# Optimization experiments

Hardware: AMD Instinct MI355X
Metric: run time of the kernel (lower is better)

## Reference

```python
import jax, jax.numpy as jnp
import numpy as np

IN_FF = 7  # joints
MASK = np.ones(9, dtype=np.float32)  # [P(3), RPY sin/cos (6)]


def _mlp(x, params):
    # params: list of (W, b); sigmoid after every layer except the last (predict)
    h = x
    for W, b in params[:-1]:
        h = jax.nn.sigmoid(h @ W + b)
    W, b = params[-1]
    return h @ W + b


def _rpy_head(x, params):
    # FeedForwardNet_RPY forward: y -> [sin(y0), cos(y1)], angle = atan2(sin, cos)
    y = _mlp(x, params)
    s = jnp.sin(y[..., 0])
    c = jnp.cos(y[..., 1])
    ang = jnp.arctan2(s, c)
    return jnp.stack([s, c, ang], axis=-1)  # (..., 3)


def setup_inputs():
    key = jax.random.key(0)
    ks = jax.random.split(key, 26)
    m = 16384
    d = {"x": jax.random.normal(ks[0], (m, 2 * IN_FF), jnp.float32)}

    def lin(k, fi, fo, name, i):
        k1, k2 = jax.random.split(k)
        lim = 1.0 / np.sqrt(fi)  # torch Linear default init
        d[name + "_W" + str(i)] = jax.random.uniform(k1, (fi, fo), jnp.float32, -lim, lim)
        d[name + "_b" + str(i)] = jax.random.uniform(k2, (fo,), jnp.float32, -lim, lim)

    idx = 1
    for name, dims in [("pos", [7, 512, 512, 3]), ("roll", [7, 256, 256, 2]),
                       ("pitch", [7, 256, 256, 2]), ("yaw", [7, 256, 256, 2])]:
        for i in range(3):
            lin(ks[idx], dims[i], dims[i + 1], name, i)
            idx += 1
    return d


def _forward(x, pos_p, roll_p, pitch_p, yaw_p):
    mask = jnp.asarray(MASK)
    M_P, M_RPY = mask[:3], mask[3:]
    q, qdot = x[:, :IN_FF], x[:, IN_FF:]

    # position net: forward + per-sample Jacobian (exact, replaces the autograd loop)
    P = _mlp(q, pos_p)                                          # (m, 3)
    J_P = jax.vmap(jax.jacfwd(lambda z: _mlp(z, pos_p)))(q)     # (m, 3, 7)
    vel = jnp.einsum("moi,mi->mo", J_P, qdot)                   # bmm(J_P, jointVels)
    P = P * M_P
    vel = vel * M_P

    heads = []
    for p in (roll_p, pitch_p, yaw_p):
        f = lambda z, p=p: _rpy_head(z, p)
        y = f(q)                                # (m, 3): [sin, cos, angle]
        J = jax.vmap(jax.jacfwd(f))(q)          # (m, 3, 7)
        v = jnp.einsum("moi,mi->mo", J[:, :2, :], qdot)  # (m, 2)
        heads.append((y, J, v))
    (yR, JR, vR), (yPi, JPi, vPi), (yY, JY, vY) = heads

    # order: [roll_sin, pitch_sin, yaw_sin, roll_cos, pitch_cos, yaw_cos]
    RPY = jnp.stack([yR[:, 0], yPi[:, 0], yY[:, 0], yR[:, 1], yPi[:, 1], yY[:, 1]], axis=1) * M_RPY
    vel_RPY = jnp.stack([vR[:, 0], vPi[:, 0], vY[:, 0], vR[:, 1], vPi[:, 1], vY[:, 1]], axis=1) * M_RPY
    J_RPY = jnp.stack([JR[:, 0], JPi[:, 0], JY[:, 0], JR[:, 1], JPi[:, 1], JY[:, 1]], axis=1)  # (m,6,7)

    out = jnp.concatenate([P, RPY, vel, vel_RPY], axis=1)            # (m, 18)
    J_tot = jnp.concatenate([J_P, J_RPY], axis=1)                    # (m, 9, 7)
    out_angles = jnp.concatenate([P, yR[:, 2:3], yPi[:, 2:3], yY[:, 2:3]], axis=1)       # (m, 6)
    J_tot_angles = jnp.concatenate([J_P, JR[:, 2:3], JPi[:, 2:3], JY[:, 2:3]], axis=1)   # (m, 6, 7)
    return out, J_tot, out_angles, J_tot_angles


def reference(x, pos_W0, pos_b0, pos_W1, pos_b1, pos_W2, pos_b2,
              roll_W0, roll_b0, roll_W1, roll_b1, roll_W2, roll_b2,
              pitch_W0, pitch_b0, pitch_W1, pitch_b1, pitch_W2, pitch_b2,
              yaw_W0, yaw_b0, yaw_W1, yaw_b1, yaw_W2, yaw_b2):
    pos_p = [(pos_W0, pos_b0), (pos_W1, pos_b1), (pos_W2, pos_b2)]
    roll_p = [(roll_W0, roll_b0), (roll_W1, roll_b1), (roll_W2, roll_b2)]
    pitch_p = [(pitch_W0, pitch_b0), (pitch_W1, pitch_b1), (pitch_W2, pitch_b2)]
    yaw_p = [(yaw_W0, yaw_b0), (yaw_W1, yaw_b1), (yaw_W2, yaw_b2)]
    return _forward(x, pos_p, roll_p, pitch_p, yaw_p)
```

## Files before the change

### kernel.cpp

```cpp
#include <hip/hip_runtime.h>
#include <math.h>

typedef __attribute__((ext_vector_type(8))) short short8;
typedef __attribute__((ext_vector_type(4))) float floatx4;

__device__ __forceinline__ float sig(float z) { return 1.0f / (1.0f + __expf(-z)); }

__device__ __forceinline__ unsigned short f2bf(float f) {
    unsigned u = __float_as_uint(f);
    u = (u + 0x7FFFu + ((u >> 16) & 1u)) >> 16;
    return (unsigned short)u;
}

__global__ void convert_w1(const float* __restrict__ src, unsigned short* __restrict__ dst,
                           int H, int logH) {
    int idx = blockIdx.x * 256 + threadIdx.x;
    if (idx >= H * H) return;
    int n = idx & (H - 1), k = idx >> logH;
    int KT = H >> 5;
    int blk = (n >> 4) * KT + (k >> 5);
    int lane = ((k >> 3) & 3) * 16 + (n & 15);
    int j = k & 7;
    dst[(blk * 64 + lane) * 8 + j] = f2bf(src[idx]);
}

struct PosS {
    float B0[512], B1[512], W2[1536];
    float Q[8][8], Qd[8][8];
    float Acc[4][64][3], Sum[64][3];
};
struct RpyS {
    float B0[256], B1[256], W2[512];
    float Q[16][8], Qd[16][8];
    float Acc[4][128][2], Sum[128][2];
};

__global__ __launch_bounds__(256, 2)
void fused_mfma(const float* __restrict__ x,
                const float* __restrict__ pW0, const float* __restrict__ pb0,
                const float* __restrict__ pb1,
                const float* __restrict__ pW2, const float* __restrict__ pb2,
                const float* __restrict__ rW0_, const float* __restrict__ rb0_,
                const float* __restrict__ rb1_,
                const float* __restrict__ rW2_, const float* __restrict__ rb2_,
                const float* __restrict__ piW0, const float* __restrict__ pib0,
                const float* __restrict__ pib1,
                const float* __restrict__ piW2, const float* __restrict__ pib2,
                const float* __restrict__ yW0, const float* __restrict__ yb0,
                const float* __restrict__ yb1,
                const float* __restrict__ yW2, const float* __restrict__ yb2,
                const unsigned short* __restrict__ wsBase,
                float* __restrict__ out, int ns)
{
    extern __shared__ unsigned short sA[];
    __shared__ union { PosS p; RpyS r; } sU;

    const int tid = threadIdx.x;
    const int f = blockIdx.x;
    const int g = f / 5, r5 = f % 5;
    const size_t JTOT = (size_t)ns * 18, OUTA = (size_t)ns * 81, JANG = (size_t)ns * 87;
    const floatx4 z4 = {0.f, 0.f, 0.f, 0.f};
    const int w = tid >> 6, lane = tid & 63;
    const int quad = lane >> 4, col = lane & 15;
    const int srcl = lane & 47;

    if (r5 < 2) {
        const int m0 = (g * 2 + r5) * 8;
        const unsigned short* wsW1 = wsBase;

        for (int i = tid; i < 512;  i += 256) { sU.p.B0[i] = pb0[i]; sU.p.B1[i] = pb1[i]; }
        for (int i = tid; i < 1536; i += 256) sU.p.W2[i] = pW2[i];
        if (tid < 112) {
            int m = tid / 14, c = tid % 14;
            float v = x[(m0 + m) * 14 + c];
            if (c < 7) sU.p.Q[m][c] = v; else sU.p.Qd[m][c - 7] = v;
        }
        __syncthreads();

        const float4* W04 = (const float4*)pW0;
        #pragma unroll
        for (int t = 0; t < 2; ++t) {
            int item = tid + t * 256;
            int s = item >> 6, k8 = item & 63;
            float q[7], w0v[7][8];
            #pragma unroll
            for (int i = 0; i < 7; i++) {
                q[i] = sU.p.Q[s][i];
                float4 a = W04[i * 128 + k8 * 2], b4 = W04[i * 128 + k8 * 2 + 1];
                w0v[i][0]=a.x; w0v[i][1]=a.y; w0v[i][2]=a.z; w0v[i][3]=a.w;
                w0v[i][4]=b4.x; w0v[i][5]=b4.y; w0v[i][6]=b4.z; w0v[i][7]=b4.w;
            }
            float hv[8], dv[8];
            #pragma unroll
            for (int jj = 0; jj < 8; jj++) {
                float z = sU.p.B0[k8 * 8 + jj];
                #pragma unroll
                for (int i = 0; i < 7; i++) z = fmaf(q[i], w0v[i][jj], z);
                float h = sig(z);
                hv[jj] = h; dv[jj] = h - h * h;
            }
            int kt = k8 >> 2, kq = k8 & 3, sw = kt & 7;
            int rr0 = s * 8;
            {
                short8 v;
                #pragma unroll
                for (int jj = 0; jj < 8; jj++) v[jj] = (short)f2bf(hv[jj]);
                *(short8*)&sA[((rr0 >> 4) * 16 + kt) * 512 + ((kq * 16 + (rr0 & 15)) ^ sw) * 8] = v;
            }
            #pragma unroll
            for (int i = 0; i < 7; i++) {
                int rr = rr0 + 1 + i;
                short8 v;
                #pragma unroll
                for (int jj = 0; jj < 8; jj++) v[jj] = (short)f2bf(dv[jj] * w0v[i][jj]);
                *(short8*)&sA[((rr >> 4) * 16 + kt) * 512 + ((kq * 16 + (rr & 15)) ^ sw) * 8] = v;
            }
        }
        __syncthreads();

        floatx4 acc[4][8];
        #pragma unroll
        for (int rt = 0; rt < 4; rt++)
            #pragma unroll
            for (int ct = 0; ct < 8; ct++) acc[rt][ct] = z4;

        const short8* bbase = (const short8*)wsW1 + (size_t)(w * 8 * 16) * 64 + lane;
        short8 bufA[8], bufB[8];
        #pragma unroll
        for (int ct = 0; ct < 8; ++ct) bufA[ct] = bbase[(ct * 16) * 64];

        for (int kt2 = 0; kt2 < 16; kt2 += 2) {
            #pragma unroll
            for (int ct = 0; ct < 8; ++ct) bufB[ct] = bbase[(ct * 16 + kt2 + 1) * 64];
            {
                const int kt = kt2, sw = kt & 7;
                short8 afr[4];
                #pragma unroll
                for (int rt = 0; rt < 4; ++rt)
                    afr[rt] = *(const short8*)&sA[(rt * 16 + kt) * 512 + (lane ^ sw) * 8];
                #pragma unroll
                for (int ct = 0; ct < 8; ++ct)
                    #pragma unroll
                    for (int rt = 0; rt < 4; ++rt)
                        acc[rt][ct] = __builtin_amdgcn_mfma_f32_16x16x32_bf16(afr[rt], bufA[ct], acc[rt][ct], 0, 0, 0);
            }
            if (kt2 + 2 < 16) {
                #pragma unroll
                for (int ct = 0; ct < 8; ++ct) bufA[ct] = bbase[(ct * 16 + kt2 + 2) * 64];
            }
            {
                const int kt = kt2 + 1, sw = kt & 7;
                short8 afr[4];
                #pragma unroll
                for (int rt = 0; rt < 4; ++rt)
                    afr[rt] = *(const short8*)&sA[(rt * 16 + kt) * 512 + (lane ^ sw) * 8];
                #pragma unroll
                for (int ct = 0; ct < 8; ++ct)
                    #pragma unroll
                    for (int rt = 0; rt < 4; ++rt)
                        acc[rt][ct] = __builtin_amdgcn_mfma_f32_16x16x32_bf16(afr[rt], bufB[ct], acc[rt][ct], 0, 0, 0);
            }
        }

        float ep[4][4][3];
        #pragma unroll
        for (int a = 0; a < 4; a++) for (int b = 0; b < 4; b++) for (int c = 0; c < 3; c++) ep[a][b][c] = 0.f;

        #pragma unroll
        for (int ct = 0; ct < 8; ++ct) {
            const int n = w * 128 + ct * 16 + col;
            const float b1n = sU.p.B1[n];
            const float w20 = sU.p.W2[n * 3], w21 = sU.p.W2[n * 3 + 1], w22 = sU.p.W2[n * 3 + 2];
            #pragma unroll
            for (int rt = 0; rt < 4; ++rt) {
                float z2c = __shfl(acc[rt][ct][0], srcl);
                float h2 = sig(z2c + b1n);
                float d2 = h2 - h2 * h2;
                #pragma unroll
                for (int r = 0; r < 4; ++r) {
                    float gg = ((quad & 1) == 0 && r == 0) ? h2 : d2 * acc[rt][ct][r];
                    ep[rt][r][0] = fmaf(gg, w20, ep[rt][r][0]);
                    ep[rt][r][1] = fmaf(gg, w21, ep[rt][r][1]);
                    ep[rt][r][2] = fmaf(gg, w22, ep[rt][r][2]);
                }
            }
        }

        #pragma unroll
        for (int mask = 1; mask <= 8; mask <<= 1)
            #pragma unroll
            for (int a = 0; a < 4; a++)
                #pragma unroll
                for (int b = 0; b < 4; b++)
                    #pragma unroll
                    for (int c = 0; c < 3; c++)
                        ep[a][b][c] += __shfl_xor(ep[a][b][c], mask);
        if (col == 0) {
            #pragma unroll
            for (int rt = 0; rt < 4; ++rt)
                #pragma unroll
                for (int r = 0; r < 4; ++r) {
                    int row = rt * 16 + quad * 4 + r;
                    sU.p.Acc[w][row][0] = ep[rt][r][0];
                    sU.p.Acc[w][row][1] = ep[rt][r][1];
                    sU.p.Acc[w][row][2] = ep[rt][r][2];
                }
        }
        __syncthreads();

        if (tid < 192) {
            int row = tid / 3, j = tid % 3;
            float v = sU.p.Acc[0][row][j] + sU.p.Acc[1][row][j] + sU.p.Acc[2][row][j] + sU.p.Acc[3][row][j];
            int s = row >> 3, i = row & 7;
            size_t M = m0 + s;
            if (i == 0) { v += pb2[j]; out[M * 18 + j] = v; out[OUTA + M * 6 + j] = v; }
            else        { out[JTOT + M * 63 + j * 7 + (i - 1)] = v;
                          out[JANG + M * 42 + j * 7 + (i - 1)] = v; }
            sU.p.Sum[row][j] = v;
        }
        __syncthreads();
        if (tid < 24) {
            int s = tid / 3, j = tid % 3;
            float vel = 0.f;
            #pragma unroll
            for (int i = 0; i < 7; i++) vel = fmaf(sU.p.Sum[s * 8 + 1 + i][j], sU.p.Qd[s][i], vel);
            out[(size_t)(m0 + s) * 18 + 9 + j] = vel;
        }
    } else {
        const int h = r5 - 2;
        const int m0 = g * 16;
        const float* W0 = (h == 0) ? rW0_ : (h == 1) ? piW0 : yW0;
        const float* b0 = (h == 0) ? rb0_ : (h == 1) ? pib0 : yb0;
        const float* b1 = (h == 0) ? rb1_ : (h == 1) ? pib1 : yb1;
        const float* W2 = (h == 0) ? rW2_ : (h == 1) ? piW2 : yW2;
        const float* b2 = (h == 0) ? rb2_ : (h == 1) ? pib2 : yb2;
        const unsigned short* wsW1 = wsBase + 262144 + h * 65536;

        if (tid < 256) { sU.r.B0[tid] = b0[tid]; sU.r.B1[tid] = b1[tid]; }
        for (int i = tid; i < 512; i += 256) sU.r.W2[i] = W2[i];
        if (tid < 224) {
            int m = tid / 14, c = tid % 14;
            float v = x[(m0 + m) * 14 + c];
            if (c < 7) sU.r.Q[m][c] = v; else sU.r.Qd[m][c - 7] = v;
        }
        __syncthreads();

        const float4* W04 = (const float4*)W0;
        #pragma unroll
        for (int t = 0; t < 2; ++t) {
            int item = tid + t * 256;
            int s = item >> 5, k8 = item & 31;
            float q[7], w0v[7][8];
            #pragma unroll
            for (int i = 0; i < 7; i++) {
                q[i] = sU.r.Q[s][i];
                float4 a = W04[i * 64 + k8 * 2], b4 = W04[i * 64 + k8 * 2 + 1];
                w0v[i][0]=a.x; w0v[i][1]=a.y; w0v[i][2]=a.z; w0v[i][3]=a.w;
                w0v[i][4]=b4.x; w0v[i][5]=b4.y; w0v[i][6]=b4.z; w0v[i][7]=b4.w;
            }
            float hv[8], dv[8];
            #pragma unroll
            for (int jj = 0; jj < 8; jj++) {
                float z = sU.r.B0[k8 * 8 + jj];
                #pragma unroll
                for (int i = 0; i < 7; i++) z = fmaf(q[i], w0v[i][jj], z);
                float hh = sig(z);
                hv[jj] = hh; dv[jj] = hh - hh * hh;
            }
            int kt = k8 >> 2, kq = k8 & 3, sw = kt & 7;
            int rr0 = s * 8;
            {
                short8 v;
                #pragma unroll
                for (int jj = 0; jj < 8; jj++) v[jj] = (short)f2bf(hv[jj]);
                *(short8*)&sA[((rr0 >> 4) * 8 + kt) * 512 + ((kq * 16 + (rr0 & 15)) ^ sw) * 8] = v;
            }
            #pragma unroll
            for (int i = 0; i < 7; i++) {
                int rr = rr0 + 1 + i;
                short8 v;
                #pragma unroll
                for (int jj = 0; jj < 8; jj++) v[jj] = (short)f2bf(dv[jj] * w0v[i][jj]);
                *(short8*)&sA[((rr >> 4) * 8 + kt) * 512 + ((kq * 16 + (rr & 15)) ^ sw) * 8] = v;
            }
        }
        __syncthreads();

        floatx4 acc[8][4];
        #pragma unroll
        for (int rt = 0; rt < 8; rt++)
            #pragma unroll
            for (int ct = 0; ct < 4; ct++) acc[rt][ct] = z4;

        const short8* bbase = (const short8*)wsW1 + (size_t)(w * 4 * 8) * 64 + lane;
        short8 bufA[4], bufB[4];
        #pragma unroll
        for (int ct = 0; ct < 4; ++ct) bufA[ct] = bbase[(ct * 8) * 64];

        for (int kt2 = 0; kt2 < 8; kt2 += 2) {
            #pragma unroll
            for (int ct = 0; ct < 4; ++ct) bufB[ct] = bbase[(ct * 8 + kt2 + 1) * 64];
            {
                const int kt = kt2, sw = kt & 7;
                short8 afr[8];
                #pragma unroll
                for (int rt = 0; rt < 8; ++rt)
                    afr[rt] = *(const short8*)&sA[(rt * 8 + kt) * 512 + (lane ^ sw) * 8];
                #pragma unroll
                for (int ct = 0; ct < 4; ++ct)
                    #pragma unroll
                    for (int rt = 0; rt < 8; ++rt)
                        acc[rt][ct] = __builtin_amdgcn_mfma_f32_16x16x32_bf16(afr[rt], bufA[ct], acc[rt][ct], 0, 0, 0);
            }
            if (kt2 + 2 < 8) {
                #pragma unroll
                for (int ct = 0; ct < 4; ++ct) bufA[ct] = bbase[(ct * 8 + kt2 + 2) * 64];
            }
            {
                const int kt = kt2 + 1, sw = kt & 7;
                short8 afr[8];
                #pragma unroll
                for (int rt = 0; rt < 8; ++rt)
                    afr[rt] = *(const short8*)&sA[(rt * 8 + kt) * 512 + (lane ^ sw) * 8];
                #pragma unroll
                for (int ct = 0; ct < 4; ++ct)
                    #pragma unroll
                    for (int rt = 0; rt < 8; ++rt)
                        acc[rt][ct] = __builtin_amdgcn_mfma_f32_16x16x32_bf16(afr[rt], bufB[ct], acc[rt][ct], 0, 0, 0);
            }
        }

        float ep[8][4][2];
        #pragma unroll
        for (int a = 0; a < 8; a++) for (int b = 0; b < 4; b++) for (int c = 0; c < 2; c++) ep[a][b][c] = 0.f;

        #pragma unroll
        for (int ct = 0; ct < 4; ++ct) {
            const int n = w * 64 + ct * 16 + col;
            const float b1n = sU.r.B1[n];
            const float w20 = sU.r.W2[n * 2], w21 = sU.r.W2[n * 2 + 1];
            #pragma unroll
            for (int rt = 0; rt < 8; ++rt) {
                float z2c = __shfl(acc[rt][ct][0], srcl);
                float h2 = sig(z2c + b1n);
                float d2 = h2 - h2 * h2;
                #pragma unroll
                for (int r = 0; r < 4; ++r) {
                    float gg = ((quad & 1) == 0 && r == 0) ? h2 : d2 * acc[rt][ct][r];
                    ep[rt][r][0] = fmaf(gg, w20, ep[rt][r][0]);
                    ep[rt][r][1] = fmaf(gg, w21, ep[rt][r][1]);
                }
            }
        }

        #pragma unroll
        for (int mask = 1; mask <= 8; mask <<= 1)
            #pragma unroll
            for (int a = 0; a < 8; a++)
                #pragma unroll
                for (int b = 0; b < 4; b++)
                    #pragma unroll
                    for (int c = 0; c < 2; c++)
                        ep[a][b][c] += __shfl_xor(ep[a][b][c], mask);
        if (col == 0) {
            #pragma unroll
            for (int rt = 0; rt < 8; ++rt)
                #pragma unroll
                for (int r = 0; r < 4; ++r) {
                    int row = rt * 16 + quad * 4 + r;
                    sU.r.Acc[w][row][0] = ep[rt][r][0];
                    sU.r.Acc[w][row][1] = ep[rt][r][1];
                }
        }
        __syncthreads();

        if (tid < 256) {
            int row = tid >> 1, j = tid & 1;
            float v = sU.r.Acc[0][row][j] + sU.r.Acc[1][row][j] + sU.r.Acc[2][row][j] + sU.r.Acc[3][row][j];
            if ((row & 7) == 0) v += b2[j];
            sU.r.Sum[row][j] = v;
        }
        __syncthreads();

        if (tid < 16) {
            int s = tid;
            size_t M = m0 + s;
            float y0 = sU.r.Sum[s * 8][0], y1 = sU.r.Sum[s * 8][1];
            float sv = sinf(y0), cv = cosf(y1);
            out[M * 18 + 3 + h] = sv;
            out[M * 18 + 6 + h] = cv;
            out[OUTA + M * 6 + 3 + h] = atan2f(sv, cv);
            float f0 = cosf(y0), f1 = -sinf(y1);
            float inv = 1.0f / fmaf(sv, sv, cv * cv);
            float v0 = 0.f, v1 = 0.f;
            #pragma unroll
            for (int i = 0; i < 7; i++) {
                float r0 = f0 * sU.r.Sum[s * 8 + 1 + i][0];
                float r1 = f1 * sU.r.Sum[s * 8 + 1 + i][1];
                out[JTOT + M * 63 + (3 + h) * 7 + i] = r0;
                out[JTOT + M * 63 + (6 + h) * 7 + i] = r1;
                out[JANG + M * 42 + (3 + h) * 7 + i] = (cv * r0 - sv * r1) * inv;
                v0 = fmaf(r0, sU.r.Qd[s][i], v0);
                v1 = fmaf(r1, sU.r.Qd[s][i], v1);
            }
            out[M * 18 + 12 + h] = v0;
            out[M * 18 + 15 + h] = v1;
        }
    }
}

extern "C" void kernel_launch(void* const* d_in, const int* in_sizes, int n_in,
                              void* d_out, int out_size, void* d_ws, size_t ws_size,
                              hipStream_t stream) {
    (void)n_in; (void)out_size; (void)ws_size;
    const float* x = (const float*)d_in[0];
    float* out = (float*)d_out;
    unsigned short* ws = (unsigned short*)d_ws;
    const int ns = in_sizes[0] / 14;

    convert_w1<<<dim3((512 * 512) / 256), 256, 0, stream>>>((const float*)d_in[3],  ws,          512, 9);
    convert_w1<<<dim3((256 * 256) / 256), 256, 0, stream>>>((const float*)d_in[9],  ws + 262144, 256, 8);
    convert_w1<<<dim3((256 * 256) / 256), 256, 0, stream>>>((const float*)d_in[15], ws + 327680, 256, 8);
    convert_w1<<<dim3((256 * 256) / 256), 256, 0, stream>>>((const float*)d_in[21], ws + 393216, 256, 8);

    fused_mfma<<<dim3((ns / 8 / 2) * 5), 256, 65536, stream>>>(
        x,
        (const float*)d_in[1],  (const float*)d_in[2],  (const float*)d_in[4],
        (const float*)d_in[5],  (const float*)d_in[6],
        (const float*)d_in[7],  (const float*)d_in[8],  (const float*)d_in[10],
        (const float*)d_in[11], (const float*)d_in[12],
        (const float*)d_in[13], (const float*)d_in[14], (const float*)d_in[16],
        (const float*)d_in[17], (const float*)d_in[18],
        (const float*)d_in[19], (const float*)d_in[20], (const float*)d_in[22],
        (const float*)d_in[23], (const float*)d_in[24],
        ws, out, ns);
}
```

Before: 335.9 us.

## Merge weight conversion launches, use packed bf16 conversion and fast reciprocals

```diff
diff --git a/kernel.cpp b/kernel.cpp
--- a/kernel.cpp
+++ b/kernel.cpp
@@ -4,7 +4,9 @@
 typedef __attribute__((ext_vector_type(8))) short short8;
 typedef __attribute__((ext_vector_type(4))) float floatx4;
 
-__device__ __forceinline__ float sig(float z) { return 1.0f / (1.0f + __expf(-z)); }
+__device__ __forceinline__ float sig(float z) {
+    return __builtin_amdgcn_rcpf(1.0f + __expf(-z));
+}
 
 __device__ __forceinline__ unsigned short f2bf(float f) {
     unsigned u = __float_as_uint(f);
@@ -12,16 +14,39 @@
     return (unsigned short)u;
 }
 
-__global__ void convert_w1(const float* __restrict__ src, unsigned short* __restrict__ dst,
-                           int H, int logH) {
+#if __has_builtin(__builtin_amdgcn_cvt_pk_bf16_f32)
+typedef __attribute__((ext_vector_type(2))) short short2v;
+__device__ __forceinline__ unsigned int pack2bf(float a, float b) {
+    short2v r = __builtin_amdgcn_cvt_pk_bf16_f32(a, b);
+    return *(unsigned int*)&r;
+}
+#else
+__device__ __forceinline__ unsigned int pack2bf(float a, float b) {
+    unsigned ua = __float_as_uint(a), ub = __float_as_uint(b);
+    ua += 0x7FFFu + ((ua >> 16) & 1u);
+    ub += 0x7FFFu + ((ub >> 16) & 1u);
+    return __builtin_amdgcn_perm(ub, ua, 0x07060302);
+}
+#endif
+
+__global__ void convert_all(const float* __restrict__ s0, const float* __restrict__ s1,
+                            const float* __restrict__ s2, const float* __restrict__ s3,
+                            unsigned short* __restrict__ ws) {
     int idx = blockIdx.x * 256 + threadIdx.x;
-    if (idx >= H * H) return;
-    int n = idx & (H - 1), k = idx >> logH;
+    const float* src; unsigned short* dst; int H, logH, local;
+    if (idx < 262144) { src = s0; dst = ws; H = 512; logH = 9; local = idx; }
+    else {
+        int r = idx - 262144; int m = r >> 16; local = r & 65535;
+        H = 256; logH = 8;
+        src = (m == 0) ? s1 : (m == 1) ? s2 : s3;
+        dst = ws + 262144 + m * 65536;
+    }
+    int n = local & (H - 1), k = local >> logH;
     int KT = H >> 5;
     int blk = (n >> 4) * KT + (k >> 5);
     int lane = ((k >> 3) & 3) * 16 + (n & 15);
     int j = k & 7;
-    dst[(blk * 64 + lane) * 8 + j] = f2bf(src[idx]);
+    dst[(blk * 64 + lane) * 8 + j] = f2bf(src[local]);
 }
 
 struct PosS {
@@ -68,8 +93,11 @@
         const int m0 = (g * 2 + r5) * 8;
         const unsigned short* wsW1 = wsBase;
 
-        for (int i = tid; i < 512;  i += 256) { sU.p.B0[i] = pb0[i]; sU.p.B1[i] = pb1[i]; }
-        for (int i = tid; i < 1536; i += 256) sU.p.W2[i] = pW2[i];
+        if (tid < 128) {
+            ((float4*)sU.p.B0)[tid] = ((const float4*)pb0)[tid];
+            ((float4*)sU.p.B1)[tid] = ((const float4*)pb1)[tid];
+        }
+        for (int i = tid; i < 384; i += 256) ((float4*)sU.p.W2)[i] = ((const float4*)pW2)[i];
         if (tid < 112) {
             int m = tid / 14, c = tid % 14;
             float v = x[(m0 + m) * 14 + c];
@@ -102,18 +130,20 @@
             int kt = k8 >> 2, kq = k8 & 3, sw = kt & 7;
             int rr0 = s * 8;
             {
-                short8 v;
-                #pragma unroll
-                for (int jj = 0; jj < 8; jj++) v[jj] = (short)f2bf(hv[jj]);
-                *(short8*)&sA[((rr0 >> 4) * 16 + kt) * 512 + ((kq * 16 + (rr0 & 15)) ^ sw) * 8] = v;
+                uint4 v;
+                v.x = pack2bf(hv[0], hv[1]); v.y = pack2bf(hv[2], hv[3]);
+                v.z = pack2bf(hv[4], hv[5]); v.w = pack2bf(hv[6], hv[7]);
+                *(uint4*)&sA[((rr0 >> 4) * 16 + kt) * 512 + ((kq * 16 + (rr0 & 15)) ^ sw) * 8] = v;
             }
             #pragma unroll
             for (int i = 0; i < 7; i++) {
                 int rr = rr0 + 1 + i;
-                short8 v;
-                #pragma unroll
-                for (int jj = 0; jj < 8; jj++) v[jj] = (short)f2bf(dv[jj] * w0v[i][jj]);
-                *(short8*)&sA[((rr >> 4) * 16 + kt) * 512 + ((kq * 16 + (rr & 15)) ^ sw) * 8] = v;
+                uint4 v;
+                v.x = pack2bf(dv[0] * w0v[i][0], dv[1] * w0v[i][1]);
+                v.y = pack2bf(dv[2] * w0v[i][2], dv[3] * w0v[i][3]);
+                v.z = pack2bf(dv[4] * w0v[i][4], dv[5] * w0v[i][5]);
+                v.w = pack2bf(dv[6] * w0v[i][6], dv[7] * w0v[i][7]);
+                *(uint4*)&sA[((rr >> 4) * 16 + kt) * 512 + ((kq * 16 + (rr & 15)) ^ sw) * 8] = v;
             }
         }
         __syncthreads();
@@ -236,8 +266,12 @@
         const float* b2 = (h == 0) ? rb2_ : (h == 1) ? pib2 : yb2;
         const unsigned short* wsW1 = wsBase + 262144 + h * 65536;
 
-        if (tid < 256) { sU.r.B0[tid] = b0[tid]; sU.r.B1[tid] = b1[tid]; }
-        for (int i = tid; i < 512; i += 256) sU.r.W2[i] = W2[i];
+        if (tid < 64) {
+            ((float4*)sU.r.B0)[tid] = ((const float4*)b0)[tid];
+            ((float4*)sU.r.B1)[tid] = ((const float4*)b1)[tid];
+        } else if (tid < 192) {
+            ((float4*)sU.r.W2)[tid - 64] = ((const float4*)W2)[tid - 64];
+        }
         if (tid < 224) {
             int m = tid / 14, c = tid % 14;
             float v = x[(m0 + m) * 14 + c];
@@ -270,18 +304,20 @@
             int kt = k8 >> 2, kq = k8 & 3, sw = kt & 7;
             int rr0 = s * 8;
             {
-                short8 v;
-                #pragma unroll
-                for (int jj = 0; jj < 8; jj++) v[jj] = (short)f2bf(hv[jj]);
-                *(short8*)&sA[((rr0 >> 4) * 8 + kt) * 512 + ((kq * 16 + (rr0 & 15)) ^ sw) * 8] = v;
+                uint4 v;
+                v.x = pack2bf(hv[0], hv[1]); v.y = pack2bf(hv[2], hv[3]);
+                v.z = pack2bf(hv[4], hv[5]); v.w = pack2bf(hv[6], hv[7]);
+                *(uint4*)&sA[((rr0 >> 4) * 8 + kt) * 512 + ((kq * 16 + (rr0 & 15)) ^ sw) * 8] = v;
             }
             #pragma unroll
             for (int i = 0; i < 7; i++) {
                 int rr = rr0 + 1 + i;
-                short8 v;
-                #pragma unroll
-                for (int jj = 0; jj < 8; jj++) v[jj] = (short)f2bf(dv[jj] * w0v[i][jj]);
-                *(short8*)&sA[((rr >> 4) * 8 + kt) * 512 + ((kq * 16 + (rr & 15)) ^ sw) * 8] = v;
+                uint4 v;
+                v.x = pack2bf(dv[0] * w0v[i][0], dv[1] * w0v[i][1]);
+                v.y = pack2bf(dv[2] * w0v[i][2], dv[3] * w0v[i][3]);
+                v.z = pack2bf(dv[4] * w0v[i][4], dv[5] * w0v[i][5]);
+                v.w = pack2bf(dv[6] * w0v[i][6], dv[7] * w0v[i][7]);
+                *(uint4*)&sA[((rr >> 4) * 8 + kt) * 512 + ((kq * 16 + (rr & 15)) ^ sw) * 8] = v;
             }
         }
         __syncthreads();
@@ -391,7 +427,7 @@
             out[M * 18 + 6 + h] = cv;
             out[OUTA + M * 6 + 3 + h] = atan2f(sv, cv);
             float f0 = cosf(y0), f1 = -sinf(y1);
-            float inv = 1.0f / fmaf(sv, sv, cv * cv);
+            float inv = __builtin_amdgcn_rcpf(fmaf(sv, sv, cv * cv));
             float v0 = 0.f, v1 = 0.f;
             #pragma unroll
             for (int i = 0; i < 7; i++) {
@@ -418,10 +454,9 @@
     unsigned short* ws = (unsigned short*)d_ws;
     const int ns = in_sizes[0] / 14;
 
-    convert_w1<<<dim3((512 * 512) / 256), 256, 0, stream>>>((const float*)d_in[3],  ws,          512, 9);
-    convert_w1<<<dim3((256 * 256) / 256), 256, 0, stream>>>((const float*)d_in[9],  ws + 262144, 256, 8);
-    convert_w1<<<dim3((256 * 256) / 256), 256, 0, stream>>>((const float*)d_in[15], ws + 327680, 256, 8);
-    convert_w1<<<dim3((256 * 256) / 256), 256, 0, stream>>>((const float*)d_in[21], ws + 393216, 256, 8);
+    convert_all<<<dim3(1792), 256, 0, stream>>>(
+        (const float*)d_in[3], (const float*)d_in[9],
+        (const float*)d_in[15], (const float*)d_in[21], ws);
 
     fused_mfma<<<dim3((ns / 8 / 2) * 5), 256, 65536, stream>>>(
         x,
```

New measurement: 341.7 us. No clear change (+1.7%).
